# Kernel tuning notes

Measured on AMD Instinct MI355X. Metric: run time of the kernel, lower is better.

Reference implementation:

```python
import jax, jax.numpy as jnp
import numpy as np

N = 100000
E = 1600000
D = 256

def setup_inputs() -> dict:
    key = jax.random.key(0)
    k1, k2, k3 = jax.random.split(key, 3)
    nodes = jax.random.normal(k1, (N, D), dtype=jnp.float32)
    edge_index = jax.random.randint(k2, (2, E), 0, N, dtype=jnp.int64)
    W = jax.random.normal(k3, (D, D), dtype=jnp.float32) * 0.05  # GCN lin weight [out,in]
    b = jnp.zeros((D,), dtype=jnp.float32)
    gamma = jnp.ones((D,), dtype=jnp.float32)
    beta = jnp.zeros((D,), dtype=jnp.float32)
    return {"nodes": nodes, "edge_index": edge_index, "W": W, "b": b,
            "gamma": gamma, "beta": beta}

def reference(nodes, edge_index, W, b, gamma, beta):
    n = nodes.shape[0]
    loop = jnp.arange(n, dtype=edge_index.dtype)
    src = jnp.concatenate([edge_index[0], loop])  # add self-loops (PyG default)
    dst = jnp.concatenate([edge_index[1], loop])
    # linear transform
    x = nodes @ W.T  # [N, D]
    # symmetric normalization: deg from target index, weight 1 per edge
    deg = jnp.zeros((n,), dtype=x.dtype).at[dst].add(1.0)
    dinv = jnp.where(deg > 0, jax.lax.rsqrt(deg), 0.0)
    norm = dinv[src] * dinv[dst]  # [E+N]
    msg = x[src] * norm[:, None]
    out = jax.ops.segment_sum(msg, dst, num_segments=n) + b  # [N, D]
    # LayerNorm over feature dim
    mu = jnp.mean(out, axis=-1, keepdims=True)
    var = jnp.mean(jnp.square(out - mu), axis=-1, keepdims=True)
    out = (out - mu) * jax.lax.rsqrt(var + 1e-5) * gamma + beta
    # ReLU; dropout is identity in eval mode
    return jax.nn.relu(out)
```

## Files before the change

### kernel.cpp

```cpp
#include <hip/hip_runtime.h>
#include <hip/hip_bf16.h>

#define NN 100000
#define EE 1600000
#define DD 256
#define CAP 48
#define NPART 782
#define PSH 7
#define PMASK 127
#define ABLK 800
#define ACHUNK 2000
#define GGRID 640
#define GT 6250

typedef __bf16 bf16x8 __attribute__((ext_vector_type(8)));
typedef float f32x4 __attribute__((ext_vector_type(4)));
typedef float f32x2 __attribute__((ext_vector_type(2)));

__device__ __forceinline__ unsigned short f2bf(float f) {
    unsigned u = __builtin_bit_cast(unsigned, f);
    u += 0x7fffu + ((u >> 16) & 1u);
    return (unsigned short)(u >> 16);
}
__device__ __forceinline__ float bf2f(unsigned short h) {
    unsigned u = ((unsigned)h) << 16;
    return __builtin_bit_cast(float, u);
}
__device__ __forceinline__ unsigned cvtpk(float a, float b) {
    unsigned r;
    asm("v_cvt_pk_bf16_f32 %0, %1, %2" : "=v"(r) : "v"(a), "v"(b));
    return r;
}

__global__ __launch_bounds__(256) void k_partA(const void* __restrict__ eptr,
        unsigned int* __restrict__ gseg2, int* __restrict__ cnts, int* __restrict__ pref,
        const float* __restrict__ W, unsigned short* __restrict__ wf) {
    __shared__ int lcnt[NPART];
    __shared__ int lcnt2[NPART];
    __shared__ int lpref[NPART];
    __shared__ int sA[1024], sB[1024];
    __shared__ __align__(16) unsigned int stash[ACHUNK];
    __shared__ unsigned short stashp[ACHUNK];
    __shared__ __align__(16) unsigned int sorted[ACHUNK];
    __shared__ int lflag;
    const int b = blockIdx.x, tid = threadIdx.x;
    if (tid == 0) lflag = 0;
    for (int i = tid; i < NPART; i += 256) { lcnt[i] = 0; lcnt2[i] = 0; }
    __syncthreads();
    if (tid < 64) {
        const unsigned long long w = ((const unsigned long long*)eptr)[tid];
        if (w > 0xFFFFFFFFULL) lflag = 1;
    }
    __syncthreads();
    const int is32 = lflag;
    const int e0 = b * ACHUNK;
    for (int e = e0 + tid; e < e0 + ACHUNK; e += 256) {
        int ss, dd;
        if (is32) { const int* p = (const int*)eptr; ss = p[e]; dd = p[EE + e]; }
        else { const long long* p = (const long long*)eptr; ss = (int)p[e]; dd = (int)p[EE + e]; }
        const int li = e - e0;
        stash[li]  = ((unsigned)ss << PSH) | (unsigned)(dd & PMASK);
        stashp[li] = (unsigned short)(dd >> PSH);
        atomicAdd(&lcnt[dd >> PSH], 1);
    }
    __syncthreads();
    for (int i = tid; i < 1024; i += 256) sA[i] = (i < NPART) ? lcnt[i] : 0;
    __syncthreads();
    int* s = sA; int* d2 = sB;
    for (int off = 1; off < 1024; off <<= 1) {
        #pragma unroll
        for (int k = 0; k < 4; ++k) {
            const int i = k * 256 + tid;
            d2[i] = s[i] + (i >= off ? s[i - off] : 0);
        }
        __syncthreads();
        int* t = s; s = d2; d2 = t;
    }
    for (int i = tid; i < NPART; i += 256) {
        lpref[i] = (i == 0) ? 0 : s[i - 1];
        cnts[(size_t)i * ABLK + b] = lcnt[i];
        pref[(size_t)i * ABLK + b] = (i == 0) ? 0 : s[i - 1];
    }
    __syncthreads();
    for (int li = tid; li < ACHUNK; li += 256) {
        const unsigned int w = stash[li];
        const int pp = stashp[li];
        const int slot = atomicAdd(&lcnt2[pp], 1);
        sorted[lpref[pp] + slot] = w;
    }
    __syncthreads();
    for (int li4 = tid; li4 < ACHUNK / 4; li4 += 256)
        *(uint4*)(gseg2 + (size_t)b * ACHUNK + (size_t)li4 * 4) = *(const uint4*)&sorted[li4 * 4];

    if (b < 32) {
        const int sl = b * 256 + tid;
        const int lane = sl & 63;
        const int ks = (sl >> 6) & 7;
        const int g  = (sl >> 9) & 3;
        const int wv = sl >> 11;
        const int feat = wv * 64 + g * 16 + (lane & 15);
        const int k0 = ks * 32 + (lane >> 4) * 8;
        const float* wp = W + (size_t)feat * 256 + k0;
        unsigned short o[8];
        #pragma unroll
        for (int j = 0; j < 8; ++j) o[j] = f2bf(wp[j]);
        uint4 pk;
        pk.x = o[0] | ((unsigned)o[1] << 16); pk.y = o[2] | ((unsigned)o[3] << 16);
        pk.z = o[4] | ((unsigned)o[5] << 16); pk.w = o[6] | ((unsigned)o[7] << 16);
        *(uint4*)(wf + (size_t)sl * 8) = pk;
    }
}

__global__ __launch_bounds__(512) void k_partB(const unsigned int* __restrict__ gseg2,
        const int* __restrict__ cnts, const int* __restrict__ pref,
        int* __restrict__ bucket, int* __restrict__ cnt) {
    __shared__ int lc[128];
    __shared__ __align__(16) int lb[128 * CAP];
    const int p = blockIdx.x, tid = threadIdx.x;
    if (tid < 128) {
        lc[tid] = 1;
        lb[tid * CAP] = p * 128 + tid;
    }
    __syncthreads();
    for (int bb = tid; bb < ABLK; bb += 512) {
        const int c = cnts[(size_t)p * ABLK + bb];
        const unsigned int* seg = gseg2 + (size_t)bb * ACHUNK + pref[(size_t)p * ABLK + bb];
        for (int i = 0; i < c; ++i) {
            const unsigned int en = seg[i];
            const int d = en & PMASK;
            const int slot = atomicAdd(&lc[d], 1);
            if (slot < CAP) lb[d * CAP + slot] = (int)(en >> PSH);
        }
    }
    __syncthreads();
    const size_t base = (size_t)p * 128 * CAP;
    #pragma unroll
    for (int it = 0; it < (128 * CAP / 4) / 512; ++it) {
        const int idx4 = it * 512 + tid;
        const int node = p * 128 + idx4 / (CAP / 4);
        if (node < NN)
            *(uint4*)(bucket + base + (size_t)idx4 * 4) = *(const uint4*)&lb[idx4 * 4];
    }
    if (tid < 128 && p * 128 + tid < NN) cnt[p * 128 + tid] = lc[tid];
}

__global__ void k_detect(const unsigned long long* __restrict__ e64, int* __restrict__ flag) {
    if (threadIdx.x == 0 && blockIdx.x == 0) {
        int is32 = 0;
        for (int i = 0; i < 64; ++i)
            if (e64[i] > 0xFFFFFFFFULL) is32 = 1;
        *flag = is32;
    }
}
__global__ __launch_bounds__(256) void k_init(int* __restrict__ cnt, int* __restrict__ bucket) {
    int v = blockIdx.x * 256 + threadIdx.x;
    if (v < NN) { cnt[v] = 1; bucket[(size_t)v * CAP] = v; }
}
__global__ __launch_bounds__(256) void k_count_scatter(const void* __restrict__ eptr,
        const int* __restrict__ flag, int* __restrict__ cnt, int* __restrict__ bucket) {
    int e = blockIdx.x * 256 + threadIdx.x;
    if (e >= EE) return;
    int s, d;
    if (*flag) { const int* p = (const int*)eptr; s = p[e]; d = p[EE + e]; }
    else { const long long* p = (const long long*)eptr; s = (int)p[e]; d = (int)p[EE + e]; }
    int slot = atomicAdd(&cnt[d], 1);
    if (slot < CAP) bucket[(size_t)d * CAP + slot] = s;
}

__global__ __launch_bounds__(256) void k_wconv(const float* __restrict__ W,
        unsigned short* __restrict__ wf) {
    const int s = blockIdx.x * 256 + threadIdx.x;
    const int lane = s & 63;
    const int ks = (s >> 6) & 7;
    const int g  = (s >> 9) & 3;
    const int wv = s >> 11;
    const int feat = wv * 64 + g * 16 + (lane & 15);
    const int k0 = ks * 32 + (lane >> 4) * 8;
    const float* wp = W + (size_t)feat * 256 + k0;
    unsigned short o[8];
    #pragma unroll
    for (int j = 0; j < 8; ++j) o[j] = f2bf(wp[j]);
    uint4 pk;
    pk.x = o[0] | ((unsigned)o[1] << 16); pk.y = o[2] | ((unsigned)o[3] << 16);
    pk.z = o[4] | ((unsigned)o[5] << 16); pk.w = o[6] | ((unsigned)o[7] << 16);
    *(uint4*)(wf + (size_t)s * 8) = pk;
}

__global__ __launch_bounds__(256, 2) void k_gemm(const float* __restrict__ nodes,
        const unsigned short* __restrict__ wf, const int* __restrict__ cnt,
        unsigned short* __restrict__ y) {
    const int tid = threadIdx.x, lane = tid & 63, wv = tid >> 6;
    const int q = lane >> 4, n0 = lane & 15;

    bf16x8 afrag[8][4];
    #pragma unroll
    for (int g = 0; g < 4; ++g)
        #pragma unroll
        for (int ks = 0; ks < 8; ++ks)
            afrag[ks][g] = *(const bf16x8*)(wf + ((((size_t)wv * 4 + g) * 8 + ks) * 64 + lane) * 8);

    for (int t = blockIdx.x; t < GT; t += GGRID) {
        const int node = t * 16 + n0;
        const float* xr = nodes + (size_t)node * 256 + q * 8;
        float4 L[16];
        #pragma unroll
        for (int ks = 0; ks < 8; ++ks) {
            L[ks * 2]     = *(const float4*)(xr + ks * 32);
            L[ks * 2 + 1] = *(const float4*)(xr + ks * 32 + 4);
        }
        const int cA = cnt[node];

        f32x4 acc[4] = {{0,0,0,0},{0,0,0,0},{0,0,0,0},{0,0,0,0}};
        #pragma unroll
        for (int ks = 0; ks < 8; ++ks) {
            uint4 u;
            u.x = cvtpk(L[ks * 2].x,     L[ks * 2].y);
            u.y = cvtpk(L[ks * 2].z,     L[ks * 2].w);
            u.z = cvtpk(L[ks * 2 + 1].x, L[ks * 2 + 1].y);
            u.w = cvtpk(L[ks * 2 + 1].z, L[ks * 2 + 1].w);
            const bf16x8 xf = __builtin_bit_cast(bf16x8, u);
            #pragma unroll
            for (int g = 0; g < 4; ++g)
                acc[g] = __builtin_amdgcn_mfma_f32_16x16x32_bf16(afrag[ks][g], xf, acc[g], 0, 0, 0);
        }

        const float dv = rsqrtf((float)cA);
        unsigned short* yp = y + (size_t)node * 256 + wv * 64 + q * 4;
        #pragma unroll
        for (int g = 0; g < 4; ++g) {
            uint2 pk;
            pk.x = cvtpk(acc[g][0] * dv, acc[g][1] * dv);
            pk.y = cvtpk(acc[g][2] * dv, acc[g][3] * dv);
            *(uint2*)(yp + g * 16) = pk;
        }
    }
}

__global__ __launch_bounds__(256) void k_gather(const unsigned short* __restrict__ y,
        const int* __restrict__ cnt, const int* __restrict__ bucket,
        const float* __restrict__ bias, const float* __restrict__ gamma,
        const float* __restrict__ beta, float* __restrict__ out) {
    const int v = blockIdx.x * 4 + (threadIdx.x >> 6);
    const int lane = threadIdx.x & 63;
    const int h = lane >> 5, l = lane & 31;
    const int c = cnt[v];
    const int my = (lane < CAP) ? bucket[(size_t)v * CAP + lane] : 0;
    const int m = min(c, CAP);

    f32x2 a2[4] = {{0,0},{0,0},{0,0},{0,0}};
    #define ACCUM(P) do {                                                      \
        a2[0] += (f32x2){__builtin_bit_cast(float, (P).x << 16),               \
                         __builtin_bit_cast(float, (P).x & 0xffff0000u)};      \
        a2[1] += (f32x2){__builtin_bit_cast(float, (P).y << 16),               \
                         __builtin_bit_cast(float, (P).y & 0xffff0000u)};      \
        a2[2] += (f32x2){__builtin_bit_cast(float, (P).z << 16),               \
                         __builtin_bit_cast(float, (P).z & 0xffff0000u)};      \
        a2[3] += (f32x2){__builtin_bit_cast(float, (P).w << 16),               \
                         __builtin_bit_cast(float, (P).w & 0xffff0000u)};      \
    } while (0)

    int j = 0;
    uint4 P0 = {0,0,0,0}, P1 = {0,0,0,0}, P2 = {0,0,0,0}, P3 = {0,0,0,0};
    const bool have8 = (m >= 8);
    if (have8) {
        const int s0 = __shfl(my, 0 + h), s1 = __shfl(my, 2 + h);
        const int s2 = __shfl(my, 4 + h), s3 = __shfl(my, 6 + h);
        P0 = *((const uint4*)(y + (size_t)s0 * 256) + l);
        P1 = *((const uint4*)(y + (size_t)s1 * 256) + l);
        P2 = *((const uint4*)(y + (size_t)s2 * 256) + l);
        P3 = *((const uint4*)(y + (size_t)s3 * 256) + l);
    }
    for (; j + 16 <= m; j += 8) {
        const int s0 = __shfl(my, j + 8 + h),  s1 = __shfl(my, j + 10 + h);
        const int s2 = __shfl(my, j + 12 + h), s3 = __shfl(my, j + 14 + h);
        const uint4 q0 = *((const uint4*)(y + (size_t)s0 * 256) + l);
        const uint4 q1 = *((const uint4*)(y + (size_t)s1 * 256) + l);
        const uint4 q2 = *((const uint4*)(y + (size_t)s2 * 256) + l);
        const uint4 q3 = *((const uint4*)(y + (size_t)s3 * 256) + l);
        ACCUM(P0); ACCUM(P1); ACCUM(P2); ACCUM(P3);
        P0 = q0; P1 = q1; P2 = q2; P3 = q3;
    }
    if (have8) {
        ACCUM(P0); ACCUM(P1); ACCUM(P2); ACCUM(P3);
        j += 8;
    }
    for (; j + 4 <= m; j += 4) {
        const int s0 = __shfl(my, j + h);
        const int s1 = __shfl(my, j + 2 + h);
        const uint4 p0 = *((const uint4*)(y + (size_t)s0 * 256) + l);
        const uint4 p1 = *((const uint4*)(y + (size_t)s1 * 256) + l);
        ACCUM(p0); ACCUM(p1);
    }
    for (; j + 2 <= m; j += 2) {
        const int s0 = __shfl(my, j + h);
        const uint4 p0 = *((const uint4*)(y + (size_t)s0 * 256) + l);
        ACCUM(p0);
    }
    if (j < m) {
        const int st = __shfl(my, j);
        if (h == 0) {
            const uint4 p0 = *((const uint4*)(y + (size_t)st * 256) + l);
            ACCUM(p0);
        }
    }
    #undef ACCUM

    float acc[8];
    acc[0] = a2[0].x; acc[1] = a2[0].y; acc[2] = a2[1].x; acc[3] = a2[1].y;
    acc[4] = a2[2].x; acc[5] = a2[2].y; acc[6] = a2[3].x; acc[7] = a2[3].y;

    #pragma unroll
    for (int i = 0; i < 8; ++i) acc[i] += __shfl_xor(acc[i], 32);

    const float dvv = rsqrtf((float)c);
    const float4 b0 = *(const float4*)(bias + l * 8);
    const float4 b1 = *(const float4*)(bias + l * 8 + 4);
    float u[8];
    u[0] = acc[0] * dvv + b0.x; u[1] = acc[1] * dvv + b0.y;
    u[2] = acc[2] * dvv + b0.z; u[3] = acc[3] * dvv + b0.w;
    u[4] = acc[4] * dvv + b1.x; u[5] = acc[5] * dvv + b1.y;
    u[6] = acc[6] * dvv + b1.z; u[7] = acc[7] * dvv + b1.w;

    float s1 = 0, s2 = 0;
    #pragma unroll
    for (int i = 0; i < 8; ++i) { s1 += u[i]; s2 += u[i] * u[i]; }
    #pragma unroll
    for (int o = 16; o > 0; o >>= 1) {
        s1 += __shfl_xor(s1, o);
        s2 += __shfl_xor(s2, o);
    }
    const float mean = s1 * (1.0f / 256.0f);
    const float var  = s2 * (1.0f / 256.0f) - mean * mean;
    const float rstd = rsqrtf(var + 1e-5f);

    const float4 g0 = *(const float4*)(gamma + l * 8);
    const float4 g1 = *(const float4*)(gamma + l * 8 + 4);
    const float4 e0 = *(const float4*)(beta + l * 8);
    const float4 e1 = *(const float4*)(beta + l * 8 + 4);
    float o8[8];
    o8[0] = fmaxf(0.0f, (u[0] - mean) * rstd * g0.x + e0.x);
    o8[1] = fmaxf(0.0f, (u[1] - mean) * rstd * g0.y + e0.y);
    o8[2] = fmaxf(0.0f, (u[2] - mean) * rstd * g0.z + e0.z);
    o8[3] = fmaxf(0.0f, (u[3] - mean) * rstd * g0.w + e0.w);
    o8[4] = fmaxf(0.0f, (u[4] - mean) * rstd * g1.x + e1.x);
    o8[5] = fmaxf(0.0f, (u[5] - mean) * rstd * g1.y + e1.y);
    o8[6] = fmaxf(0.0f, (u[6] - mean) * rstd * g1.z + e1.z);
    o8[7] = fmaxf(0.0f, (u[7] - mean) * rstd * g1.w + e1.w);
    float4 ov;
    if (h == 0) { ov.x = o8[0]; ov.y = o8[1]; ov.z = o8[2]; ov.w = o8[3]; }
    else        { ov.x = o8[4]; ov.y = o8[5]; ov.z = o8[6]; ov.w = o8[7]; }
    *(float4*)(out + (size_t)v * 256 + l * 8 + h * 4) = ov;
}

extern "C" void kernel_launch(void* const* d_in, const int* in_sizes, int n_in,
                              void* d_out, int out_size, void* d_ws, size_t ws_size,
                              hipStream_t stream) {
    const float* nodes = (const float*)d_in[0];
    const void*  edges = d_in[1];
    const float* W     = (const float*)d_in[2];
    const float* b     = (const float*)d_in[3];
    const float* gamma = (const float*)d_in[4];
    const float* beta  = (const float*)d_in[5];
    float* out = (float*)d_out;

    char* ws = (char*)d_ws;
    size_t off = 0;
    auto alloc = [&](size_t bytes) { size_t p = off; off = (off + bytes + 255) & ~(size_t)255; return p; };
    int*            cnt    = (int*)(ws + alloc((size_t)NN * 4));
    int*            flag   = (int*)(ws + alloc(256));
    int*            bucket = (int*)(ws + alloc((size_t)NN * CAP * 4));
    unsigned short* y      = (unsigned short*)(ws + alloc((size_t)NN * DD * 2));
    unsigned short* wf     = (unsigned short*)(ws + alloc((size_t)DD * DD * 2));
    int*            cnts   = (int*)(ws + alloc((size_t)NPART * ABLK * 4));
    int*            pref   = (int*)(ws + alloc((size_t)NPART * ABLK * 4));
    unsigned int*   gseg2  = (unsigned int*)(ws + alloc((size_t)EE * 4));
    const size_t full_need = off;
    (void)in_sizes; (void)n_in; (void)out_size;

    if (ws_size >= full_need) {
        k_partA<<<ABLK, 256, 0, stream>>>(edges, gseg2, cnts, pref, W, wf);
        k_partB<<<NPART, 512, 0, stream>>>(gseg2, cnts, pref, bucket, cnt);
    } else {
        k_wconv<<<32, 256, 0, stream>>>(W, wf);
        k_detect<<<1, 64, 0, stream>>>((const unsigned long long*)edges, flag);
        k_init<<<(NN + 255) / 256, 256, 0, stream>>>(cnt, bucket);
        k_count_scatter<<<(EE + 255) / 256, 256, 0, stream>>>(edges, flag, cnt, bucket);
    }
    k_gemm<<<GGRID, 256, 0, stream>>>(nodes, wf, cnt, y);
    k_gather<<<NN / 4, 256, 0, stream>>>(y, cnt, bucket, b, gamma, beta, out);
}
```

Measured before the change: 433.9 us.

## Pipeline GEMM tile loads through LDS double buffer and pack partition metadata

The GEMM kernel now handles 32-node tiles. Each tile is loaded with coalesced row-contiguous float4 reads, converted to bf16 and staged into a double-buffered LDS array. The global load for a tile two steps ahead is issued while the current tile's MFMAs run. This targets the exposed global load latency and poor coalescing of the per-lane strided loads, at the cost of extra LDS traffic, barriers and register pressure. Separately, the edge partitioning uses fewer, larger chunks (500 blocks of 3200 edges) with counts and prefixes packed into one int2 array, so partB makes one load per chunk with a single pass per thread.

```diff
diff --git a/kernel.cpp b/kernel.cpp
--- a/kernel.cpp
+++ b/kernel.cpp
@@ -8,10 +8,10 @@
 #define NPART 782
 #define PSH 7
 #define PMASK 127
-#define ABLK 800
-#define ACHUNK 2000
-#define GGRID 640
-#define GT 6250
+#define ABLK 500
+#define ACHUNK 3200
+#define GTILES 3125
+#define GGRID 512
 
 typedef __bf16 bf16x8 __attribute__((ext_vector_type(8)));
 typedef float f32x4 __attribute__((ext_vector_type(4)));
@@ -33,7 +33,7 @@
 }
 
 __global__ __launch_bounds__(256) void k_partA(const void* __restrict__ eptr,
-        unsigned int* __restrict__ gseg2, int* __restrict__ cnts, int* __restrict__ pref,
+        unsigned int* __restrict__ gseg2, int2* __restrict__ cp,
         const float* __restrict__ W, unsigned short* __restrict__ wf) {
     __shared__ int lcnt[NPART];
     __shared__ int lcnt2[NPART];
@@ -77,9 +77,9 @@
         int* t = s; s = d2; d2 = t;
     }
     for (int i = tid; i < NPART; i += 256) {
-        lpref[i] = (i == 0) ? 0 : s[i - 1];
-        cnts[(size_t)i * ABLK + b] = lcnt[i];
-        pref[(size_t)i * ABLK + b] = (i == 0) ? 0 : s[i - 1];
+        const int pv = (i == 0) ? 0 : s[i - 1];
+        lpref[i] = pv;
+        cp[(size_t)i * ABLK + b] = make_int2(lcnt[i], pv);
     }
     __syncthreads();
     for (int li = tid; li < ACHUNK; li += 256) {
@@ -112,8 +112,7 @@
 }
 
 __global__ __launch_bounds__(512) void k_partB(const unsigned int* __restrict__ gseg2,
-        const int* __restrict__ cnts, const int* __restrict__ pref,
-        int* __restrict__ bucket, int* __restrict__ cnt) {
+        const int2* __restrict__ cp, int* __restrict__ bucket, int* __restrict__ cnt) {
     __shared__ int lc[128];
     __shared__ __align__(16) int lb[128 * CAP];
     const int p = blockIdx.x, tid = threadIdx.x;
@@ -122,10 +121,10 @@
         lb[tid * CAP] = p * 128 + tid;
     }
     __syncthreads();
-    for (int bb = tid; bb < ABLK; bb += 512) {
-        const int c = cnts[(size_t)p * ABLK + bb];
-        const unsigned int* seg = gseg2 + (size_t)bb * ACHUNK + pref[(size_t)p * ABLK + bb];
-        for (int i = 0; i < c; ++i) {
+    if (tid < ABLK) {
+        const int2 v = cp[(size_t)p * ABLK + tid];
+        const unsigned int* seg = gseg2 + (size_t)tid * ACHUNK + v.y;
+        for (int i = 0; i < v.x; ++i) {
             const unsigned int en = seg[i];
             const int d = en & PMASK;
             const int slot = atomicAdd(&lc[d], 1);
@@ -189,8 +188,11 @@
 __global__ __launch_bounds__(256, 2) void k_gemm(const float* __restrict__ nodes,
         const unsigned short* __restrict__ wf, const int* __restrict__ cnt,
         unsigned short* __restrict__ y) {
+    __shared__ __align__(16) unsigned short xlds[2][32][264];
     const int tid = threadIdx.x, lane = tid & 63, wv = tid >> 6;
     const int q = lane >> 4, n0 = lane & 15;
+    const int r_ = tid >> 6;
+    const int c4 = tid & 63;
 
     bf16x8 afrag[8][4];
     #pragma unroll
@@ -199,41 +201,91 @@
         for (int ks = 0; ks < 8; ++ks)
             afrag[ks][g] = *(const bf16x8*)(wf + ((((size_t)wv * 4 + g) * 8 + ks) * 64 + lane) * 8);
 
-    for (int t = blockIdx.x; t < GT; t += GGRID) {
-        const int node = t * 16 + n0;
-        const float* xr = nodes + (size_t)node * 256 + q * 8;
-        float4 L[16];
-        #pragma unroll
-        for (int ks = 0; ks < 8; ++ks) {
-            L[ks * 2]     = *(const float4*)(xr + ks * 32);
-            L[ks * 2 + 1] = *(const float4*)(xr + ks * 32 + 4);
+#define LOADT(R, TT) do {                                                      \
+    const float* src_ = nodes + (size_t)(TT) * 32 * 256;                       \
+    _Pragma("unroll")                                                          \
+    for (int rr = 0; rr < 8; ++rr)                                             \
+        R[rr] = *(const float4*)(src_ + (size_t)(rr * 4 + r_) * 256 + c4 * 4); \
+} while (0)
+
+#define CONVW(R, BUF) do {                                                     \
+    _Pragma("unroll")                                                          \
+    for (int rr = 0; rr < 8; ++rr) {                                           \
+        uint2 pk_;                                                             \
+        pk_.x = cvtpk(R[rr].x, R[rr].y);                                       \
+        pk_.y = cvtpk(R[rr].z, R[rr].w);                                       \
+        *(uint2*)&xlds[BUF][rr * 4 + r_][c4 * 4] = pk_;                        \
+    }                                                                          \
+} while (0)
+
+#define COMPUTE_STORE(TT, BUF) do {                                            \
+    const int node0_ = (TT) * 32;                                              \
+    const int cA_ = cnt[node0_ + n0];                                          \
+    const int cB_ = cnt[node0_ + 16 + n0];                                     \
+    f32x4 acc_[2][4];                                                          \
+    _Pragma("unroll")                                                          \
+    for (int sub = 0; sub < 2; ++sub)                                          \
+        _Pragma("unroll")                                                      \
+        for (int g = 0; g < 4; ++g) acc_[sub][g] = (f32x4){0, 0, 0, 0};        \
+    _Pragma("unroll")                                                          \
+    for (int ks = 0; ks < 8; ++ks) {                                           \
+        _Pragma("unroll")                                                      \
+        for (int sub = 0; sub < 2; ++sub) {                                    \
+            const bf16x8 xf_ = *(const bf16x8*)&xlds[BUF][sub * 16 + n0][ks * 32 + q * 8]; \
+            _Pragma("unroll")                                                  \
+            for (int g = 0; g < 4; ++g)                                        \
+                acc_[sub][g] = __builtin_amdgcn_mfma_f32_16x16x32_bf16(afrag[ks][g], xf_, acc_[sub][g], 0, 0, 0); \
+        }                                                                      \
+    }                                                                          \
+    const float dv0_ = rsqrtf((float)cA_);                                     \
+    const float dv1_ = rsqrtf((float)cB_);                                     \
+    unsigned short* yp0_ = y + (size_t)(node0_ + n0) * 256 + wv * 64 + q * 4;  \
+    unsigned short* yp1_ = y + (size_t)(node0_ + 16 + n0) * 256 + wv * 64 + q * 4; \
+    _Pragma("unroll")                                                          \
+    for (int g = 0; g < 4; ++g) {                                              \
+        uint2 pk_;                                                             \
+        pk_.x = cvtpk(acc_[0][g][0] * dv0_, acc_[0][g][1] * dv0_);             \
+        pk_.y = cvtpk(acc_[0][g][2] * dv0_, acc_[0][g][3] * dv0_);             \
+        *(uint2*)(yp0_ + g * 16) = pk_;                                        \
+        uint2 pk1_;                                                            \
+        pk1_.x = cvtpk(acc_[1][g][0] * dv1_, acc_[1][g][1] * dv1_);            \
+        pk1_.y = cvtpk(acc_[1][g][2] * dv1_, acc_[1][g][3] * dv1_);            \
+        *(uint2*)(yp1_ + g * 16) = pk1_;                                       \
+    }                                                                          \
+} while (0)
+
+    float4 rA[8], rB[8];
+    int t = blockIdx.x;
+    int cur = 0;
+
+    LOADT(rA, t);
+    CONVW(rA, 0);
+    if (t + GGRID < GTILES) LOADT(rA, t + GGRID);
+    __syncthreads();
+
+    while (true) {
+        {
+            const int tn = t + GGRID, tn2 = t + 2 * GGRID;
+            if (tn2 < GTILES) LOADT(rB, tn2);
+            COMPUTE_STORE(t, cur);
+            if (tn >= GTILES) break;
+            CONVW(rA, cur ^ 1);
+            __syncthreads();
+            cur ^= 1; t = tn;
         }
-        const int cA = cnt[node];
-
-        f32x4 acc[4] = {{0,0,0,0},{0,0,0,0},{0,0,0,0},{0,0,0,0}};
-        #pragma unroll
-        for (int ks = 0; ks < 8; ++ks) {
-            uint4 u;
-            u.x = cvtpk(L[ks * 2].x,     L[ks * 2].y);
-            u.y = cvtpk(L[ks * 2].z,     L[ks * 2].w);
-            u.z = cvtpk(L[ks * 2 + 1].x, L[ks * 2 + 1].y);
-            u.w = cvtpk(L[ks * 2 + 1].z, L[ks * 2 + 1].w);
-            const bf16x8 xf = __builtin_bit_cast(bf16x8, u);
-            #pragma unroll
-            for (int g = 0; g < 4; ++g)
-                acc[g] = __builtin_amdgcn_mfma_f32_16x16x32_bf16(afrag[ks][g], xf, acc[g], 0, 0, 0);
+        {
+            const int tn = t + GGRID, tn2 = t + 2 * GGRID;
+            if (tn2 < GTILES) LOADT(rA, tn2);
+            COMPUTE_STORE(t, cur);
+            if (tn >= GTILES) break;
+            CONVW(rB, cur ^ 1);
+            __syncthreads();
+            cur ^= 1; t = tn;
         }
-
-        const float dv = rsqrtf((float)cA);
-        unsigned short* yp = y + (size_t)node * 256 + wv * 64 + q * 4;
-        #pragma unroll
-        for (int g = 0; g < 4; ++g) {
-            uint2 pk;
-            pk.x = cvtpk(acc[g][0] * dv, acc[g][1] * dv);
-            pk.y = cvtpk(acc[g][2] * dv, acc[g][3] * dv);
-            *(uint2*)(yp + g * 16) = pk;
-        }
-    }
+    }
+#undef LOADT
+#undef CONVW
+#undef COMPUTE_STORE
 }
 
 __global__ __launch_bounds__(256) void k_gather(const unsigned short* __restrict__ y,
@@ -371,15 +423,14 @@
     int*            bucket = (int*)(ws + alloc((size_t)NN * CAP * 4));
     unsigned short* y      = (unsigned short*)(ws + alloc((size_t)NN * DD * 2));
     unsigned short* wf     = (unsigned short*)(ws + alloc((size_t)DD * DD * 2));
-    int*            cnts   = (int*)(ws + alloc((size_t)NPART * ABLK * 4));
-    int*            pref   = (int*)(ws + alloc((size_t)NPART * ABLK * 4));
+    int2*           cp     = (int2*)(ws + alloc((size_t)NPART * ABLK * 8));
     unsigned int*   gseg2  = (unsigned int*)(ws + alloc((size_t)EE * 4));
     const size_t full_need = off;
     (void)in_sizes; (void)n_in; (void)out_size;
 
     if (ws_size >= full_need) {
-        k_partA<<<ABLK, 256, 0, stream>>>(edges, gseg2, cnts, pref, W, wf);
-        k_partB<<<NPART, 512, 0, stream>>>(gseg2, cnts, pref, bucket, cnt);
+        k_partA<<<ABLK, 256, 0, stream>>>(edges, gseg2, cp, W, wf);
+        k_partB<<<NPART, 512, 0, stream>>>(gseg2, cp, bucket, cnt);
     } else {
         k_wconv<<<32, 256, 0, stream>>>(W, wf);
         k_detect<<<1, 64, 0, stream>>>((const unsigned long long*)edges, flag);
```

Result: faster. 355.0 us (-18.2%).
